# Kernel optimization log

Measured on AMD Instinct MI355X. Metric: run time of the kernel, lower is better.

The kernel has to match this reference:

```python
import jax, jax.numpy as jnp
import numpy as np

N_NODES = 50000
N_EDGES = 800000
IN_FEAT = 64
HIDDEN = 128
NUM_LAYERS = 3


def setup_inputs() -> dict:
    key = jax.random.key(0)
    ks = jax.random.split(key, 8)
    x = jax.random.normal(ks[0], (N_NODES, IN_FEAT), dtype=jnp.float32)
    edge_index = jax.random.randint(ks[1], (2, N_EDGES), 0, N_NODES, dtype=jnp.int64)
    s_in = 1.0 / np.sqrt(IN_FEAT)
    s_h = 1.0 / np.sqrt(HIDDEN)
    W_in = jax.random.uniform(ks[2], (IN_FEAT, HIDDEN), jnp.float32, -s_in, s_in)
    b_in = jax.random.uniform(ks[3], (HIDDEN,), jnp.float32, -s_in, s_in)
    W_self = jax.random.uniform(ks[4], (NUM_LAYERS, HIDDEN, HIDDEN), jnp.float32, -s_h, s_h)
    b_self = jax.random.uniform(ks[5], (NUM_LAYERS, HIDDEN), jnp.float32, -s_h, s_h)
    W_nbr = jax.random.uniform(ks[6], (NUM_LAYERS, HIDDEN, HIDDEN), jnp.float32, -s_h, s_h)
    return {"x": x, "edge_index": edge_index, "W_in": W_in, "b_in": b_in,
            "W_self": W_self, "b_self": b_self, "W_nbr": W_nbr}


def reference(x, edge_index, W_in, b_in, W_self, b_self, W_nbr):
    # input projection: h [N, HIDDEN]
    h = x @ W_in + b_in
    src = edge_index[0]
    dst = edge_index[1]
    n = h.shape[0]
    ones = jnp.ones((dst.shape[0], 1), dtype=h.dtype)
    # scatter-mean denominator is grad-constant; compute once
    cnt = jax.ops.segment_sum(ones, dst, num_segments=n)
    cnt = jnp.maximum(cnt, 1.0)
    for l in range(W_self.shape[0]):
        msg = h[src] @ W_nbr[l]                               # [E, HIDDEN]
        agg = jax.ops.segment_sum(msg, dst, num_segments=n) / cnt  # scatter-mean
        h = jax.nn.elu(h @ W_self[l] + b_self[l] + agg)
    return h
```

## Files before the change

### kernel.cpp

```cpp
#include <hip/hip_runtime.h>
#include <cstdint>

#define HIDDEN 128

typedef unsigned short u16;
using frag_t   = __attribute__((ext_vector_type(8))) short;
using f32x4_t  = __attribute__((ext_vector_type(4))) float;
using ushort8_t = __attribute__((ext_vector_type(8))) unsigned short;

__device__ __forceinline__ float bf2f(u16 u) {
    union { unsigned int i; float f; } c;
    c.i = ((unsigned int)u) << 16;
    return c.f;
}
__device__ __forceinline__ u16 f2bf(float f) {
    unsigned int u = __float_as_uint(f);
    unsigned int r = (u + 0x7fffu + ((u >> 16) & 1u)) >> 16;
    return (u16)r;
}

__device__ __forceinline__ size_t fmaj(int row, int col, int KF) {
    int T = row >> 4, m = row & 15;
    int f = col >> 5, q = (col & 31) >> 3, j = col & 7;
    return ((size_t)(T * KF + f) * 64 + q * 16 + m) * 8 + j;
}


__global__ void k_hist(const int* __restrict__ ei, int E, int* __restrict__ deg, int npr) {
    int r  = blockIdx.x & 7;
    int lo = r * npr, hi = lo + npr;
    int nb = gridDim.x >> 3;
    int bi = blockIdx.x >> 3;
    int tid = bi * blockDim.x + threadIdx.x;
    int stride = nb * blockDim.x;
    if ((E & 3) == 0) {
        const int4* d4 = (const int4*)(ei + E);
        int nch = E >> 2;
        for (int c = tid; c < nch; c += stride) {
            int4 d = d4[c];
            if (d.x >= lo && d.x < hi) atomicAdd(&deg[d.x], 1);
            if (d.y >= lo && d.y < hi) atomicAdd(&deg[d.y], 1);
            if (d.z >= lo && d.z < hi) atomicAdd(&deg[d.z], 1);
            if (d.w >= lo && d.w < hi) atomicAdd(&deg[d.w], 1);
        }
    } else {
        for (int e = tid; e < E; e += stride) {
            int d = ei[E + e];
            if (d >= lo && d < hi) atomicAdd(&deg[d], 1);
        }
    }
}

__global__ void k_scan1(const int* __restrict__ deg, int* __restrict__ rowp,
                        int* __restrict__ bsums, int n) {
    __shared__ int sh[1024];
    int t = threadIdx.x;
    int base = blockIdx.x * 1024;
    int v = (base + t < n) ? deg[base + t] : 0;
    sh[t] = v;
    __syncthreads();
    for (int off = 1; off < 1024; off <<= 1) {
        int x = sh[t];
        int y = (t >= off) ? sh[t - off] : 0;
        __syncthreads();
        sh[t] = x + y;
        __syncthreads();
    }
    if (base + t < n) rowp[base + t + 1] = sh[t];
    if (t == 1023) bsums[blockIdx.x] = sh[1023];
}

__global__ void k_scan2(int* __restrict__ bsums, int nb) {
    int lane = threadIdx.x;
    int carry = 0;
    for (int base = 0; base < nb; base += 64) {
        int i = base + lane;
        int v = (i < nb) ? bsums[i] : 0;
        int incl = v;
#pragma unroll
        for (int off = 1; off < 64; off <<= 1) {
            int y = __shfl_up(incl, off, 64);
            if (lane >= off) incl += y;
        }
        if (i < nb) bsums[i] = carry + (incl - v);
        carry += __shfl(incl, 63, 64);
    }
}

__global__ void k_scan3(int* __restrict__ rowp, const int* __restrict__ boffs,
                        int* __restrict__ fillp, int n) {
    int t = threadIdx.x;
    int b = blockIdx.x;
    int base = b * 1024;
    if (base + t < n) {
        int v = rowp[base + t + 1] + boffs[b];
        rowp[base + t + 1] = v;
        if (base + t + 1 < n) fillp[base + t + 1] = v;
    }
    if (b == 0 && t == 0) { rowp[0] = 0; fillp[0] = 0; }
}

__global__ void k_fill(const int* __restrict__ ei, int E,
                       int* __restrict__ fillpos, int* __restrict__ colx, int npr) {
    int r  = blockIdx.x & 7;
    int lo = r * npr, hi = lo + npr;
    int nb = gridDim.x >> 3;
    int bi = blockIdx.x >> 3;
    int tid = bi * blockDim.x + threadIdx.x;
    int stride = nb * blockDim.x;
    if ((E & 3) == 0) {
        const int4* s4 = (const int4*)ei;
        const int4* d4 = (const int4*)(ei + E);
        int nch = E >> 2;
        for (int c = tid; c < nch; c += stride) {
            int4 d = d4[c];
            bool m0 = d.x >= lo && d.x < hi;
            bool m1 = d.y >= lo && d.y < hi;
            bool m2 = d.z >= lo && d.z < hi;
            bool m3 = d.w >= lo && d.w < hi;
            if (m0 | m1 | m2 | m3) {
                int4 s = s4[c];
                if (m0) colx[atomicAdd(&fillpos[d.x], 1)] = s.x;
                if (m1) colx[atomicAdd(&fillpos[d.y], 1)] = s.y;
                if (m2) colx[atomicAdd(&fillpos[d.z], 1)] = s.z;
                if (m3) colx[atomicAdd(&fillpos[d.w], 1)] = s.w;
            }
        }
    } else {
        for (int e = tid; e < E; e += stride) {
            int d = ei[E + e];
            if (d >= lo && d < hi) colx[atomicAdd(&fillpos[d], 1)] = ei[e];
        }
    }
}


__global__ void k_prep(const float* __restrict__ x,
                       const float* __restrict__ W_in,
                       const float* __restrict__ W_self,
                       const float* __restrict__ W_nbr,
                       u16* __restrict__ xf,
                       u16* __restrict__ WtI_hi, u16* __restrict__ WtI_lo,
                       u16* __restrict__ WtS_hi, u16* __restrict__ WtS_lo,
                       u16* __restrict__ WtN_hi, u16* __restrict__ WtN_lo,
                       int L, int nxg) {
    int nIn = 64 * 128;
    int nSq = L * 128 * 128;
    int wtot = nIn + 2 * nSq;
    int total = wtot + nxg;
    int stride = gridDim.x * blockDim.x;
    for (int i = blockIdx.x * blockDim.x + threadIdx.x; i < total; i += stride) {
        if (i >= wtot) {
            int t = i - wtot;
            int row = t >> 3, c = t & 7;
            const float4* xs = (const float4*)(x + (size_t)row * 64 + c * 8);
            float4 v0 = xs[0], v1 = xs[1];
            ushort8_t o;
            o[0] = f2bf(v0.x); o[1] = f2bf(v0.y); o[2] = f2bf(v0.z); o[3] = f2bf(v0.w);
            o[4] = f2bf(v1.x); o[5] = f2bf(v1.y); o[6] = f2bf(v1.z); o[7] = f2bf(v1.w);
            int T = row >> 4, m = row & 15;
            int f = c >> 2, q = c & 3;
            *(ushort8_t*)&xf[((size_t)(T * 2 + f) * 64 + q * 16 + m) * 8] = o;
        } else {
            float v; u16* phi; u16* plo; int o;
            if (i < nIn) {
                int n = i / 64, k = i % 64;
                v = W_in[k * 128 + n]; phi = WtI_hi; plo = WtI_lo; o = n * 64 + k;
            } else if (i < nIn + nSq) {
                int t = i - nIn;
                int l = t / (128 * 128), r = t % (128 * 128);
                int n = r / 128, k = r % 128;
                v = W_self[l * 128 * 128 + k * 128 + n]; phi = WtS_hi; plo = WtS_lo;
                o = l * 128 * 128 + n * 128 + k;
            } else {
                int t = i - nIn - nSq;
                int l = t / (128 * 128), r = t % (128 * 128);
                int n = r / 128, k = r % 128;
                v = W_nbr[l * 128 * 128 + k * 128 + n]; phi = WtN_hi; plo = WtN_lo;
                o = l * 128 * 128 + n * 128 + k;
            }
            u16 hi = f2bf(v);
            phi[o] = hi;
            plo[o] = f2bf(v - bf2f(hi));
        }
    }
}


__global__ __launch_bounds__(256, 4) void k_agg(
        const ushort8_t* __restrict__ hb8, const int* __restrict__ rowp,
        const int* __restrict__ colx, u16* __restrict__ Sf, int n) {
    int g = (blockIdx.x * blockDim.x + threadIdx.x) >> 4;
    int lane = threadIdx.x & 15;
    if (g >= n) return;
    int beg = rowp[g];
    int end = rowp[g + 1];
    float a0[8], a1[8];
#pragma unroll
    for (int j = 0; j < 8; ++j) { a0[j] = 0.f; a1[j] = 0.f; }
    int e = beg;
    for (; e + 7 < end; e += 8) {
        int s0 = colx[e],     s1 = colx[e + 1], s2 = colx[e + 2], s3 = colx[e + 3];
        int s4 = colx[e + 4], s5 = colx[e + 5], s6 = colx[e + 6], s7 = colx[e + 7];
        ushort8_t v0 = hb8[(size_t)s0 * 16 + lane];
        ushort8_t v1 = hb8[(size_t)s1 * 16 + lane];
        ushort8_t v2 = hb8[(size_t)s2 * 16 + lane];
        ushort8_t v3 = hb8[(size_t)s3 * 16 + lane];
        ushort8_t v4 = hb8[(size_t)s4 * 16 + lane];
        ushort8_t v5 = hb8[(size_t)s5 * 16 + lane];
        ushort8_t v6 = hb8[(size_t)s6 * 16 + lane];
        ushort8_t v7 = hb8[(size_t)s7 * 16 + lane];
#pragma unroll
        for (int j = 0; j < 8; ++j) {
            a0[j] += bf2f(v0[j]); a1[j] += bf2f(v1[j]);
            a0[j] += bf2f(v2[j]); a1[j] += bf2f(v3[j]);
            a0[j] += bf2f(v4[j]); a1[j] += bf2f(v5[j]);
            a0[j] += bf2f(v6[j]); a1[j] += bf2f(v7[j]);
        }
    }
    for (; e + 3 < end; e += 4) {
        int s0 = colx[e], s1 = colx[e + 1], s2 = colx[e + 2], s3 = colx[e + 3];
        ushort8_t v0 = hb8[(size_t)s0 * 16 + lane];
        ushort8_t v1 = hb8[(size_t)s1 * 16 + lane];
        ushort8_t v2 = hb8[(size_t)s2 * 16 + lane];
        ushort8_t v3 = hb8[(size_t)s3 * 16 + lane];
#pragma unroll
        for (int j = 0; j < 8; ++j) {
            a0[j] += bf2f(v0[j]); a1[j] += bf2f(v1[j]);
            a0[j] += bf2f(v2[j]); a1[j] += bf2f(v3[j]);
        }
    }
    for (; e < end; ++e) {
        int s = colx[e];
        ushort8_t v = hb8[(size_t)s * 16 + lane];
#pragma unroll
        for (int j = 0; j < 8; ++j) a0[j] += bf2f(v[j]);
    }
    int deg = end - beg;
    float inv = 1.0f / (float)(deg > 1 ? deg : 1);
    ushort8_t o;
#pragma unroll
    for (int j = 0; j < 8; ++j) o[j] = f2bf((a0[j] + a1[j]) * inv);
    int T = g >> 4, m = g & 15;
    *(ushort8_t*)&Sf[((size_t)(T * 4 + (lane >> 2)) * 64 + (lane & 3) * 16 + m) * 8] = o;
}


template <int KF1, int KF2, int DO_ELU>
__global__ __launch_bounds__(256, 2) void k_gemm_mfma(
    const u16* __restrict__ A1f, const u16* __restrict__ A2f,
    const u16* __restrict__ B1h, const u16* __restrict__ B1l,
    const u16* __restrict__ B2h, const u16* __restrict__ B2l,
    const float* __restrict__ bias, float* __restrict__ C,
    u16* __restrict__ Hrow, u16* __restrict__ Hf,
    int M)
{
    constexpr int K1 = KF1 * 32;
    constexpr int K2 = KF2 * 32;
    constexpr int KF = KF1 + KF2;
    int lane = threadIdx.x & 63;
    int w    = threadIdx.x >> 6;
    int m16  = lane & 15;
    int quad = lane >> 4;
    int kq   = quad * 8;
    int ng   = (blockIdx.x >> 3) & 1;
    int mtb  = (blockIdx.x & 7) | ((blockIdx.x >> 4) << 3);
    int ncol = (ng * 4 + w) * 16 + m16;

    frag_t bh[KF], bl[KF];
    if constexpr (KF1 > 0) {
#pragma unroll
        for (int f = 0; f < KF1; ++f) {
            bh[f] = *(const frag_t*)&B1h[(size_t)ncol * K1 + f * 32 + kq];
            bl[f] = *(const frag_t*)&B1l[(size_t)ncol * K1 + f * 32 + kq];
        }
    }
    if constexpr (KF2 > 0) {
#pragma unroll
        for (int f = 0; f < KF2; ++f) {
            bh[KF1 + f] = *(const frag_t*)&B2h[(size_t)ncol * K2 + f * 32 + kq];
            bl[KF1 + f] = *(const frag_t*)&B2l[(size_t)ncol * K2 + f * 32 + kq];
        }
    }

    float bv = bias[ncol];
    int nMT  = (M + 31) >> 5;
    int step = gridDim.x >> 1;
    int fcol = ncol >> 5;
    int qcol = (ncol & 31) >> 3;
    int jcol = ncol & 7;

    auto loadA = [&](int mt, frag_t (&a0)[KF], frag_t (&a1)[KF]) {
        int T0 = mt * 2, T1 = T0 + 1;
        if constexpr (KF1 > 0) {
#pragma unroll
            for (int f = 0; f < KF1; ++f) {
                a0[f] = *(const frag_t*)&A1f[((size_t)(T0 * KF1 + f) * 64 + lane) * 8];
                a1[f] = *(const frag_t*)&A1f[((size_t)(T1 * KF1 + f) * 64 + lane) * 8];
            }
        }
        if constexpr (KF2 > 0) {
#pragma unroll
            for (int f = 0; f < KF2; ++f) {
                a0[KF1 + f] = *(const frag_t*)&A2f[((size_t)(T0 * KF2 + f) * 64 + lane) * 8];
                a1[KF1 + f] = *(const frag_t*)&A2f[((size_t)(T1 * KF2 + f) * 64 + lane) * 8];
            }
        }
    };

    auto compute = [&](int mt, frag_t (&a0)[KF], frag_t (&a1)[KF]) {
        f32x4_t acc0 = (f32x4_t){0.f, 0.f, 0.f, 0.f};
        f32x4_t acc1 = (f32x4_t){0.f, 0.f, 0.f, 0.f};
#pragma unroll
        for (int f = 0; f < KF; ++f) {
            acc0 = __builtin_amdgcn_mfma_f32_16x16x32_bf16(a0[f], bh[f], acc0, 0, 0, 0);
            acc1 = __builtin_amdgcn_mfma_f32_16x16x32_bf16(a1[f], bh[f], acc1, 0, 0, 0);
            acc0 = __builtin_amdgcn_mfma_f32_16x16x32_bf16(a0[f], bl[f], acc0, 0, 0, 0);
            acc1 = __builtin_amdgcn_mfma_f32_16x16x32_bf16(a1[f], bl[f], acc1, 0, 0, 0);
        }
        int rb = mt * 32 + quad * 4;
#pragma unroll
        for (int r = 0; r < 4; ++r) {
#pragma unroll
            for (int half = 0; half < 2; ++half) {
                int row = rb + r + half * 16;
                float av = half ? acc1[r] : acc0[r];
                if (row < M) {
                    float v = av + bv;
                    if constexpr (DO_ELU) v = (v > 0.f) ? v : expm1f(v);
                    if (C) C[(size_t)row * HIDDEN + ncol] = v;
                    if (Hrow) {
                        u16 hv = f2bf(v);
                        Hrow[(size_t)row * HIDDEN + ncol] = hv;
                        Hf[((size_t)((row >> 4) * 4 + fcol) * 64 + qcol * 16 + (row & 15)) * 8 + jcol] = hv;
                    }
                }
            }
        }
    };

    int mt = mtb;
    if (mt >= nMT) return;
    frag_t xa0[KF], xa1[KF], ya0[KF], ya1[KF];
    loadA(mt, xa0, xa1);
    while (true) {
        int mt2 = mt + step;
        if (mt2 < nMT) loadA(mt2, ya0, ya1);
        compute(mt, xa0, xa1);
        if (mt2 >= nMT) break;
        int mt3 = mt2 + step;
        if (mt3 < nMT) loadA(mt3, xa0, xa1);
        compute(mt2, ya0, ya1);
        if (mt3 >= nMT) break;
        mt = mt3;
    }
}


extern "C" void kernel_launch(void* const* d_in, const int* in_sizes, int n_in,
                              void* d_out, int out_size, void* d_ws, size_t ws_size,
                              hipStream_t stream) {
    const float* x        = (const float*)d_in[0];
    const int* ei         = (const int*)d_in[1];
    const float* W_in     = (const float*)d_in[2];
    const float* b_in     = (const float*)d_in[3];
    const float* W_self   = (const float*)d_in[4];
    const float* b_self   = (const float*)d_in[5];
    const float* W_nbr    = (const float*)d_in[6];
    float* out = (float*)d_out;

    const int IN_FEAT = 64;
    int N = in_sizes[0] / IN_FEAT;
    int E = in_sizes[1] / 2;
    int L = in_sizes[4] / (HIDDEN * HIDDEN);

    char* ws = (char*)d_ws;
    size_t off = 0;
    auto alloc = [&](size_t bytes) -> void* {
        void* p = ws + off;
        off = (off + bytes + 255) & ~(size_t)255;
        return p;
    };

    int nT = ((N + 31) / 32) * 2;

    u16* hRowA = (u16*)alloc((size_t)N * HIDDEN * 2);
    u16* hRowB = (u16*)alloc((size_t)N * HIDDEN * 2);
    u16* hfA   = (u16*)alloc((size_t)nT * 4 * 64 * 8 * 2);
    u16* hfB   = (u16*)alloc((size_t)nT * 4 * 64 * 8 * 2);
    u16* xf    = (u16*)alloc((size_t)nT * 2 * 64 * 8 * 2);
    u16* Sf    = (u16*)alloc((size_t)nT * 4 * 64 * 8 * 2);
    u16* WtI_hi = (u16*)alloc(128 * 64 * 2);
    u16* WtI_lo = (u16*)alloc(128 * 64 * 2);
    u16* WtS_hi = (u16*)alloc((size_t)L * 128 * 128 * 2);
    u16* WtS_lo = (u16*)alloc((size_t)L * 128 * 128 * 2);
    u16* WtN_hi = (u16*)alloc((size_t)L * 128 * 128 * 2);
    u16* WtN_lo = (u16*)alloc((size_t)L * 128 * 128 * 2);
    int* deg   = (int*)alloc((size_t)N * sizeof(int));
    int* rowp  = (int*)alloc((size_t)(N + 1) * sizeof(int));
    int* fillp = (int*)alloc((size_t)N * sizeof(int));
    int* colx  = (int*)alloc((size_t)E * sizeof(int));
    int* bsums = (int*)alloc(256 * sizeof(int));

    int npr = (N + 7) / 8;

    hipMemsetAsync(deg, 0, (size_t)N * sizeof(int), stream);
    k_hist<<<2048, 256, 0, stream>>>(ei, E, deg, npr);
    int nb = (N + 1023) / 1024;
    k_scan1<<<nb, 1024, 0, stream>>>(deg, rowp, bsums, N);
    k_scan2<<<1, 64, 0, stream>>>(bsums, nb);
    k_scan3<<<nb, 1024, 0, stream>>>(rowp, bsums, fillp, N);
    k_fill<<<2048, 256, 0, stream>>>(ei, E, fillp, colx, npr);

    int wtot = 64 * 128 + 2 * L * 128 * 128;
    int prep_total = wtot + N * 8;
    k_prep<<<(prep_total + 255) / 256, 256, 0, stream>>>(
        x, W_in, W_self, W_nbr, xf,
        WtI_hi, WtI_lo, WtS_hi, WtS_lo, WtN_hi, WtN_lo, L, N * 8);

    const int GB = 1024;

    k_gemm_mfma<2, 0, 0><<<GB, 256, 0, stream>>>(
        xf, nullptr,
        WtI_hi, WtI_lo, nullptr, nullptr,
        b_in, nullptr, hRowA, hfA, N);

    u16* curRow = hRowA; u16* curF = hfA;
    u16* nxtRow = hRowB; u16* nxtF = hfB;

    for (int l = 0; l < L; ++l) {
        k_agg<<<(N + 15) / 16, 256, 0, stream>>>((const ushort8_t*)curRow, rowp, colx, Sf, N);
        const u16* Wsh = WtS_hi + (size_t)l * 128 * 128;
        const u16* Wsl = WtS_lo + (size_t)l * 128 * 128;
        const u16* Wnh = WtN_hi + (size_t)l * 128 * 128;
        const u16* Wnl = WtN_lo + (size_t)l * 128 * 128;
        const float* bs = b_self + (size_t)l * HIDDEN;
        bool last = (l == L - 1);
        k_gemm_mfma<4, 4, 1><<<GB, 256, 0, stream>>>(
            curF, Sf,
            Wsh, Wsl, Wnh, Wnl,
            bs, last ? out : nullptr,
            last ? nullptr : nxtRow, last ? nullptr : nxtF, N);
        u16* tr = curRow; curRow = nxtRow; nxtRow = tr;
        u16* tf = curF;   curF = nxtF;     nxtF = tf;
    }
}
```

Measured before the change: 338.9 us.

## Fuse neighbor aggregation into per-layer MFMA GEMM and collapse scan into one kernel

Adds a k_layer kernel that gathers and mean-reduces neighbor features for a 32-node tile into LDS, then runs the self and neighbor MFMA GEMM on that tile with ELU in the same kernel. This removes the separate aggregation pass and the global write and re-read of the aggregated buffer Sf, and halves launches per layer. The three-kernel prefix scan is also replaced by a single-block scan kernel. In exchange, gather latency and MFMA work are now serialized within each block, and the single-block scan runs on only one CU.

```diff
diff --git a/kernel.cpp b/kernel.cpp
--- a/kernel.cpp
+++ b/kernel.cpp
@@ -17,12 +17,6 @@
     unsigned int u = __float_as_uint(f);
     unsigned int r = (u + 0x7fffu + ((u >> 16) & 1u)) >> 16;
     return (u16)r;
-}
-
-__device__ __forceinline__ size_t fmaj(int row, int col, int KF) {
-    int T = row >> 4, m = row & 15;
-    int f = col >> 5, q = (col & 31) >> 3, j = col & 7;
-    return ((size_t)(T * KF + f) * 64 + q * 16 + m) * 8 + j;
 }
 
 
@@ -51,13 +45,16 @@
     }
 }
 
-__global__ void k_scan1(const int* __restrict__ deg, int* __restrict__ rowp,
-                        int* __restrict__ bsums, int n) {
+__global__ void k_scan_all(const int* __restrict__ deg, int* __restrict__ rowp,
+                           int* __restrict__ fillp, int n) {
     __shared__ int sh[1024];
     int t = threadIdx.x;
-    int base = blockIdx.x * 1024;
-    int v = (base + t < n) ? deg[base + t] : 0;
-    sh[t] = v;
+    int C = (n + 1023) >> 10;
+    int lo = t * C;
+    int hi = lo + C; if (hi > n) hi = n;
+    int s = 0;
+    for (int i = lo; i < hi; ++i) s += deg[i];
+    sh[t] = s;
     __syncthreads();
     for (int off = 1; off < 1024; off <<= 1) {
         int x = sh[t];
@@ -66,38 +63,13 @@
         sh[t] = x + y;
         __syncthreads();
     }
-    if (base + t < n) rowp[base + t + 1] = sh[t];
-    if (t == 1023) bsums[blockIdx.x] = sh[1023];
-}
-
-__global__ void k_scan2(int* __restrict__ bsums, int nb) {
-    int lane = threadIdx.x;
-    int carry = 0;
-    for (int base = 0; base < nb; base += 64) {
-        int i = base + lane;
-        int v = (i < nb) ? bsums[i] : 0;
-        int incl = v;
-#pragma unroll
-        for (int off = 1; off < 64; off <<= 1) {
-            int y = __shfl_up(incl, off, 64);
-            if (lane >= off) incl += y;
-        }
-        if (i < nb) bsums[i] = carry + (incl - v);
-        carry += __shfl(incl, 63, 64);
-    }
-}
-
-__global__ void k_scan3(int* __restrict__ rowp, const int* __restrict__ boffs,
-                        int* __restrict__ fillp, int n) {
-    int t = threadIdx.x;
-    int b = blockIdx.x;
-    int base = b * 1024;
-    if (base + t < n) {
-        int v = rowp[base + t + 1] + boffs[b];
-        rowp[base + t + 1] = v;
-        if (base + t + 1 < n) fillp[base + t + 1] = v;
-    }
-    if (b == 0 && t == 0) { rowp[0] = 0; fillp[0] = 0; }
+    int run = (t == 0) ? 0 : sh[t - 1];
+    for (int i = lo; i < hi; ++i) {
+        rowp[i] = run;
+        fillp[i] = run;
+        run += deg[i];
+    }
+    if (hi == n && lo <= n) rowp[n] = run;
 }
 
 __global__ void k_fill(const int* __restrict__ ei, int E,
@@ -187,77 +159,16 @@
 }
 
 
-__global__ __launch_bounds__(256, 4) void k_agg(
-        const ushort8_t* __restrict__ hb8, const int* __restrict__ rowp,
-        const int* __restrict__ colx, u16* __restrict__ Sf, int n) {
-    int g = (blockIdx.x * blockDim.x + threadIdx.x) >> 4;
-    int lane = threadIdx.x & 15;
-    if (g >= n) return;
-    int beg = rowp[g];
-    int end = rowp[g + 1];
-    float a0[8], a1[8];
-#pragma unroll
-    for (int j = 0; j < 8; ++j) { a0[j] = 0.f; a1[j] = 0.f; }
-    int e = beg;
-    for (; e + 7 < end; e += 8) {
-        int s0 = colx[e],     s1 = colx[e + 1], s2 = colx[e + 2], s3 = colx[e + 3];
-        int s4 = colx[e + 4], s5 = colx[e + 5], s6 = colx[e + 6], s7 = colx[e + 7];
-        ushort8_t v0 = hb8[(size_t)s0 * 16 + lane];
-        ushort8_t v1 = hb8[(size_t)s1 * 16 + lane];
-        ushort8_t v2 = hb8[(size_t)s2 * 16 + lane];
-        ushort8_t v3 = hb8[(size_t)s3 * 16 + lane];
-        ushort8_t v4 = hb8[(size_t)s4 * 16 + lane];
-        ushort8_t v5 = hb8[(size_t)s5 * 16 + lane];
-        ushort8_t v6 = hb8[(size_t)s6 * 16 + lane];
-        ushort8_t v7 = hb8[(size_t)s7 * 16 + lane];
-#pragma unroll
-        for (int j = 0; j < 8; ++j) {
-            a0[j] += bf2f(v0[j]); a1[j] += bf2f(v1[j]);
-            a0[j] += bf2f(v2[j]); a1[j] += bf2f(v3[j]);
-            a0[j] += bf2f(v4[j]); a1[j] += bf2f(v5[j]);
-            a0[j] += bf2f(v6[j]); a1[j] += bf2f(v7[j]);
-        }
-    }
-    for (; e + 3 < end; e += 4) {
-        int s0 = colx[e], s1 = colx[e + 1], s2 = colx[e + 2], s3 = colx[e + 3];
-        ushort8_t v0 = hb8[(size_t)s0 * 16 + lane];
-        ushort8_t v1 = hb8[(size_t)s1 * 16 + lane];
-        ushort8_t v2 = hb8[(size_t)s2 * 16 + lane];
-        ushort8_t v3 = hb8[(size_t)s3 * 16 + lane];
-#pragma unroll
-        for (int j = 0; j < 8; ++j) {
-            a0[j] += bf2f(v0[j]); a1[j] += bf2f(v1[j]);
-            a0[j] += bf2f(v2[j]); a1[j] += bf2f(v3[j]);
-        }
-    }
-    for (; e < end; ++e) {
-        int s = colx[e];
-        ushort8_t v = hb8[(size_t)s * 16 + lane];
-#pragma unroll
-        for (int j = 0; j < 8; ++j) a0[j] += bf2f(v[j]);
-    }
-    int deg = end - beg;
-    float inv = 1.0f / (float)(deg > 1 ? deg : 1);
-    ushort8_t o;
-#pragma unroll
-    for (int j = 0; j < 8; ++j) o[j] = f2bf((a0[j] + a1[j]) * inv);
-    int T = g >> 4, m = g & 15;
-    *(ushort8_t*)&Sf[((size_t)(T * 4 + (lane >> 2)) * 64 + (lane & 3) * 16 + m) * 8] = o;
-}
-
-
-template <int KF1, int KF2, int DO_ELU>
+template <int KF1, int DO_ELU>
 __global__ __launch_bounds__(256, 2) void k_gemm_mfma(
-    const u16* __restrict__ A1f, const u16* __restrict__ A2f,
+    const u16* __restrict__ A1f,
     const u16* __restrict__ B1h, const u16* __restrict__ B1l,
-    const u16* __restrict__ B2h, const u16* __restrict__ B2l,
     const float* __restrict__ bias, float* __restrict__ C,
     u16* __restrict__ Hrow, u16* __restrict__ Hf,
     int M)
 {
     constexpr int K1 = KF1 * 32;
-    constexpr int K2 = KF2 * 32;
-    constexpr int KF = KF1 + KF2;
+    constexpr int KF = KF1;
     int lane = threadIdx.x & 63;
     int w    = threadIdx.x >> 6;
     int m16  = lane & 15;
@@ -268,19 +179,10 @@
     int ncol = (ng * 4 + w) * 16 + m16;
 
     frag_t bh[KF], bl[KF];
-    if constexpr (KF1 > 0) {
-#pragma unroll
-        for (int f = 0; f < KF1; ++f) {
-            bh[f] = *(const frag_t*)&B1h[(size_t)ncol * K1 + f * 32 + kq];
-            bl[f] = *(const frag_t*)&B1l[(size_t)ncol * K1 + f * 32 + kq];
-        }
-    }
-    if constexpr (KF2 > 0) {
-#pragma unroll
-        for (int f = 0; f < KF2; ++f) {
-            bh[KF1 + f] = *(const frag_t*)&B2h[(size_t)ncol * K2 + f * 32 + kq];
-            bl[KF1 + f] = *(const frag_t*)&B2l[(size_t)ncol * K2 + f * 32 + kq];
-        }
+#pragma unroll
+    for (int f = 0; f < KF; ++f) {
+        bh[f] = *(const frag_t*)&B1h[(size_t)ncol * K1 + f * 32 + kq];
+        bl[f] = *(const frag_t*)&B1l[(size_t)ncol * K1 + f * 32 + kq];
     }
 
     float bv = bias[ncol];
@@ -292,19 +194,10 @@
 
     auto loadA = [&](int mt, frag_t (&a0)[KF], frag_t (&a1)[KF]) {
         int T0 = mt * 2, T1 = T0 + 1;
-        if constexpr (KF1 > 0) {
-#pragma unroll
-            for (int f = 0; f < KF1; ++f) {
-                a0[f] = *(const frag_t*)&A1f[((size_t)(T0 * KF1 + f) * 64 + lane) * 8];
-                a1[f] = *(const frag_t*)&A1f[((size_t)(T1 * KF1 + f) * 64 + lane) * 8];
-            }
-        }
-        if constexpr (KF2 > 0) {
-#pragma unroll
-            for (int f = 0; f < KF2; ++f) {
-                a0[KF1 + f] = *(const frag_t*)&A2f[((size_t)(T0 * KF2 + f) * 64 + lane) * 8];
-                a1[KF1 + f] = *(const frag_t*)&A2f[((size_t)(T1 * KF2 + f) * 64 + lane) * 8];
-            }
+#pragma unroll
+        for (int f = 0; f < KF; ++f) {
+            a0[f] = *(const frag_t*)&A1f[((size_t)(T0 * KF1 + f) * 64 + lane) * 8];
+            a1[f] = *(const frag_t*)&A1f[((size_t)(T1 * KF1 + f) * 64 + lane) * 8];
         }
     };
 
@@ -357,6 +250,158 @@
 }
 
 
+template <int DO_ELU>
+__global__ __launch_bounds__(512, 2) void k_layer(
+    const ushort8_t* __restrict__ hb8,
+    const u16* __restrict__ Af,
+    const int* __restrict__ rowp, const int* __restrict__ colx,
+    const u16* __restrict__ Bsh, const u16* __restrict__ Bsl,
+    const u16* __restrict__ Bnh, const u16* __restrict__ Bnl,
+    const float* __restrict__ bias,
+    float* __restrict__ C, u16* __restrict__ Hrow, u16* __restrict__ Hf,
+    int M)
+{
+    constexpr int KF1 = 4, KF2 = 4, KF = 8;
+    __shared__ u16 lds_sf[2][2 * KF2 * 64 * 8];
+
+    int tid  = threadIdx.x;
+    int lane = tid & 63;
+    int w    = tid >> 6;
+    int m16  = lane & 15;
+    int quad = lane >> 4;
+    int kq   = quad * 8;
+    int ncol = w * 16 + m16;
+
+    frag_t bh[KF], bl[KF];
+#pragma unroll
+    for (int f = 0; f < KF1; ++f) {
+        bh[f] = *(const frag_t*)&Bsh[(size_t)ncol * 128 + f * 32 + kq];
+        bl[f] = *(const frag_t*)&Bsl[(size_t)ncol * 128 + f * 32 + kq];
+    }
+#pragma unroll
+    for (int f = 0; f < KF2; ++f) {
+        bh[KF1 + f] = *(const frag_t*)&Bnh[(size_t)ncol * 128 + f * 32 + kq];
+        bl[KF1 + f] = *(const frag_t*)&Bnl[(size_t)ncol * 128 + f * 32 + kq];
+    }
+    float bv = bias[ncol];
+
+    int anode = tid >> 4;
+    int alane = tid & 15;
+    int sOff = ((((anode >> 4) * 4 + (alane >> 2)) * 64) + (alane & 3) * 16 + (anode & 15)) * 8;
+
+    int nMT  = (M + 31) >> 5;
+    int fcol = ncol >> 5;
+    int qcol = (ncol & 31) >> 3;
+    int jcol = ncol & 7;
+
+    int p = 0;
+    for (int mt = blockIdx.x; mt < nMT; mt += gridDim.x) {
+        int g = mt * 32 + anode;
+        ushort8_t o;
+        if (g < M) {
+            int beg = rowp[g];
+            int end = rowp[g + 1];
+            float a0[8], a1[8];
+#pragma unroll
+            for (int j = 0; j < 8; ++j) { a0[j] = 0.f; a1[j] = 0.f; }
+            int e = beg;
+            for (; e + 7 < end; e += 8) {
+                int s0 = colx[e],     s1 = colx[e + 1], s2 = colx[e + 2], s3 = colx[e + 3];
+                int s4 = colx[e + 4], s5 = colx[e + 5], s6 = colx[e + 6], s7 = colx[e + 7];
+                ushort8_t v0 = hb8[(size_t)s0 * 16 + alane];
+                ushort8_t v1 = hb8[(size_t)s1 * 16 + alane];
+                ushort8_t v2 = hb8[(size_t)s2 * 16 + alane];
+                ushort8_t v3 = hb8[(size_t)s3 * 16 + alane];
+                ushort8_t v4 = hb8[(size_t)s4 * 16 + alane];
+                ushort8_t v5 = hb8[(size_t)s5 * 16 + alane];
+                ushort8_t v6 = hb8[(size_t)s6 * 16 + alane];
+                ushort8_t v7 = hb8[(size_t)s7 * 16 + alane];
+#pragma unroll
+                for (int j = 0; j < 8; ++j) {
+                    a0[j] += bf2f(v0[j]); a1[j] += bf2f(v1[j]);
+                    a0[j] += bf2f(v2[j]); a1[j] += bf2f(v3[j]);
+                    a0[j] += bf2f(v4[j]); a1[j] += bf2f(v5[j]);
+                    a0[j] += bf2f(v6[j]); a1[j] += bf2f(v7[j]);
+                }
+            }
+            for (; e + 3 < end; e += 4) {
+                int s0 = colx[e], s1 = colx[e + 1], s2 = colx[e + 2], s3 = colx[e + 3];
+                ushort8_t v0 = hb8[(size_t)s0 * 16 + alane];
+                ushort8_t v1 = hb8[(size_t)s1 * 16 + alane];
+                ushort8_t v2 = hb8[(size_t)s2 * 16 + alane];
+                ushort8_t v3 = hb8[(size_t)s3 * 16 + alane];
+#pragma unroll
+                for (int j = 0; j < 8; ++j) {
+                    a0[j] += bf2f(v0[j]); a1[j] += bf2f(v1[j]);
+                    a0[j] += bf2f(v2[j]); a1[j] += bf2f(v3[j]);
+                }
+            }
+            for (; e < end; ++e) {
+                int s = colx[e];
+                ushort8_t v = hb8[(size_t)s * 16 + alane];
+#pragma unroll
+                for (int j = 0; j < 8; ++j) a0[j] += bf2f(v[j]);
+            }
+            int deg = end - beg;
+            float inv = 1.0f / (float)(deg > 1 ? deg : 1);
+#pragma unroll
+            for (int j = 0; j < 8; ++j) o[j] = f2bf((a0[j] + a1[j]) * inv);
+        } else {
+#pragma unroll
+            for (int j = 0; j < 8; ++j) o[j] = 0;
+        }
+        *(ushort8_t*)&lds_sf[p][sOff] = o;
+
+        int T0 = mt * 2, T1 = T0 + 1;
+        frag_t a0f[KF], a1f[KF];
+#pragma unroll
+        for (int f = 0; f < KF1; ++f) {
+            a0f[f] = *(const frag_t*)&Af[((size_t)(T0 * KF1 + f) * 64 + lane) * 8];
+            a1f[f] = *(const frag_t*)&Af[((size_t)(T1 * KF1 + f) * 64 + lane) * 8];
+        }
+
+        __syncthreads();
+
+#pragma unroll
+        for (int f = 0; f < KF2; ++f) {
+            a0f[KF1 + f] = *(const frag_t*)&lds_sf[p][((0 * 4 + f) * 64 + lane) * 8];
+            a1f[KF1 + f] = *(const frag_t*)&lds_sf[p][((1 * 4 + f) * 64 + lane) * 8];
+        }
+
+        f32x4_t acc0 = (f32x4_t){0.f, 0.f, 0.f, 0.f};
+        f32x4_t acc1 = (f32x4_t){0.f, 0.f, 0.f, 0.f};
+#pragma unroll
+        for (int f = 0; f < KF; ++f) {
+            acc0 = __builtin_amdgcn_mfma_f32_16x16x32_bf16(a0f[f], bh[f], acc0, 0, 0, 0);
+            acc1 = __builtin_amdgcn_mfma_f32_16x16x32_bf16(a1f[f], bh[f], acc1, 0, 0, 0);
+            acc0 = __builtin_amdgcn_mfma_f32_16x16x32_bf16(a0f[f], bl[f], acc0, 0, 0, 0);
+            acc1 = __builtin_amdgcn_mfma_f32_16x16x32_bf16(a1f[f], bl[f], acc1, 0, 0, 0);
+        }
+
+        int rb = mt * 32 + quad * 4;
+#pragma unroll
+        for (int r = 0; r < 4; ++r) {
+#pragma unroll
+            for (int half = 0; half < 2; ++half) {
+                int row = rb + r + half * 16;
+                float av = half ? acc1[r] : acc0[r];
+                if (row < M) {
+                    float v = av + bv;
+                    if constexpr (DO_ELU) v = (v > 0.f) ? v : expm1f(v);
+                    if (C) C[(size_t)row * HIDDEN + ncol] = v;
+                    if (Hrow) {
+                        u16 hv = f2bf(v);
+                        Hrow[(size_t)row * HIDDEN + ncol] = hv;
+                        Hf[((size_t)((row >> 4) * 4 + fcol) * 64 + qcol * 16 + (row & 15)) * 8 + jcol] = hv;
+                    }
+                }
+            }
+        }
+        p ^= 1;
+    }
+}
+
+
 extern "C" void kernel_launch(void* const* d_in, const int* in_sizes, int n_in,
                               void* d_out, int out_size, void* d_ws, size_t ws_size,
                               hipStream_t stream) {
@@ -389,7 +434,6 @@
     u16* hfA   = (u16*)alloc((size_t)nT * 4 * 64 * 8 * 2);
     u16* hfB   = (u16*)alloc((size_t)nT * 4 * 64 * 8 * 2);
     u16* xf    = (u16*)alloc((size_t)nT * 2 * 64 * 8 * 2);
-    u16* Sf    = (u16*)alloc((size_t)nT * 4 * 64 * 8 * 2);
     u16* WtI_hi = (u16*)alloc(128 * 64 * 2);
     u16* WtI_lo = (u16*)alloc(128 * 64 * 2);
     u16* WtS_hi = (u16*)alloc((size_t)L * 128 * 128 * 2);
@@ -400,16 +444,12 @@
     int* rowp  = (int*)alloc((size_t)(N + 1) * sizeof(int));
     int* fillp = (int*)alloc((size_t)N * sizeof(int));
     int* colx  = (int*)alloc((size_t)E * sizeof(int));
-    int* bsums = (int*)alloc(256 * sizeof(int));
 
     int npr = (N + 7) / 8;
 
     hipMemsetAsync(deg, 0, (size_t)N * sizeof(int), stream);
     k_hist<<<2048, 256, 0, stream>>>(ei, E, deg, npr);
-    int nb = (N + 1023) / 1024;
-    k_scan1<<<nb, 1024, 0, stream>>>(deg, rowp, bsums, N);
-    k_scan2<<<1, 64, 0, stream>>>(bsums, nb);
-    k_scan3<<<nb, 1024, 0, stream>>>(rowp, bsums, fillp, N);
+    k_scan_all<<<1, 1024, 0, stream>>>(deg, rowp, fillp, N);
     k_fill<<<2048, 256, 0, stream>>>(ei, E, fillp, colx, npr);
 
     int wtot = 64 * 128 + 2 * L * 128 * 128;
@@ -418,28 +458,23 @@
         x, W_in, W_self, W_nbr, xf,
         WtI_hi, WtI_lo, WtS_hi, WtS_lo, WtN_hi, WtN_lo, L, N * 8);
 
-    const int GB = 1024;
-
-    k_gemm_mfma<2, 0, 0><<<GB, 256, 0, stream>>>(
-        xf, nullptr,
-        WtI_hi, WtI_lo, nullptr, nullptr,
-        b_in, nullptr, hRowA, hfA, N);
+    k_gemm_mfma<2, 0><<<1024, 256, 0, stream>>>(
+        xf, WtI_hi, WtI_lo, b_in, nullptr, hRowA, hfA, N);
 
     u16* curRow = hRowA; u16* curF = hfA;
     u16* nxtRow = hRowB; u16* nxtF = hfB;
 
     for (int l = 0; l < L; ++l) {
-        k_agg<<<(N + 15) / 16, 256, 0, stream>>>((const ushort8_t*)curRow, rowp, colx, Sf, N);
         const u16* Wsh = WtS_hi + (size_t)l * 128 * 128;
         const u16* Wsl = WtS_lo + (size_t)l * 128 * 128;
         const u16* Wnh = WtN_hi + (size_t)l * 128 * 128;
         const u16* Wnl = WtN_lo + (size_t)l * 128 * 128;
         const float* bs = b_self + (size_t)l * HIDDEN;
         bool last = (l == L - 1);
-        k_gemm_mfma<4, 4, 1><<<GB, 256, 0, stream>>>(
-            curF, Sf,
-            Wsh, Wsl, Wnh, Wnl,
-            bs, last ? out : nullptr,
+        k_layer<1><<<512, 512, 0, stream>>>(
+            (const ushort8_t*)curRow, curF, rowp, colx,
+            Wsh, Wsl, Wnh, Wnl, bs,
+            last ? out : nullptr,
             last ? nullptr : nxtRow, last ? nullptr : nxtF, N);
         u16* tr = curRow; curRow = nxtRow; nxtRow = tr;
         u16* tf = curF;   curF = nxtF;     nxtF = tf;
```

After: 468.9 us. 38.4% more time.
